# Kernel tuning notes

Measured on AMD Instinct MI355X. Metric: run time of the kernel, lower is better.

## Reference

```python
import jax, jax.numpy as jnp
import numpy as np

FACTOR = 0.2          # rotation/zoom/shift factor (init kwarg)
SCALE = 1.0 / 255.0   # rescale (init kwarg)
TWO_PI = 6.283185307179586
B, H, W, C = 64, 224, 224, 3


def _reflect(i, n):
    # TF fill_mode='reflect' index mapping (symmetric with edge repeat)
    m = jnp.mod(i, 2 * n)
    return jnp.where(m >= n, 2 * n - 1 - m, m)


def _bilinear(img, xs, ys):
    # img [H,W,C]; xs, ys [H,W] = input-space sample coords for each output pixel
    h, w, _ = img.shape
    x0f = jnp.floor(xs)
    y0f = jnp.floor(ys)
    fx = (xs - x0f)[..., None]
    fy = (ys - y0f)[..., None]
    x0 = x0f.astype(jnp.int32)
    y0 = y0f.astype(jnp.int32)
    x0r = _reflect(x0, w); x1r = _reflect(x0 + 1, w)
    y0r = _reflect(y0, h); y1r = _reflect(y0 + 1, h)
    Ia = img[y0r, x0r]; Ib = img[y0r, x1r]
    Ic = img[y1r, x0r]; Id = img[y1r, x1r]
    top = Ia * (1.0 - fx) + Ib * fx
    bot = Ic * (1.0 - fx) + Id * fx
    return top * (1.0 - fy) + bot * fy


_warp = jax.vmap(_bilinear)  # over batch: images [B,H,W,C], coords [B,H,W]


def setup_inputs() -> dict:
    key = jax.random.key(0)
    k = jax.random.split(key, 5)
    return {
        "image": jax.random.uniform(k[0], (B, H, W, C), jnp.float32) * 255.0,
        "angle_u": jax.random.uniform(k[1], (B,), jnp.float32),
        "zoom_u": jax.random.uniform(k[2], (B, 2), jnp.float32),
        "shift_u": jax.random.uniform(k[3], (B, 2), jnp.float32),
        "flip_u": jax.random.uniform(k[4], (B,), jnp.float32),
    }


def reference(image, angle_u, zoom_u, shift_u, flip_u):
    b, h, w, _ = image.shape
    dt = image.dtype
    yy, xx = jnp.meshgrid(jnp.arange(h, dtype=dt), jnp.arange(w, dtype=dt), indexing='ij')
    cx = (w - 1) / 2.0
    cy = (h - 1) / 2.0

    # 1) rescale
    x = image * SCALE

    # 2) random rotation: angle uniform in [-factor*2pi, +factor*2pi]
    theta = (2.0 * angle_u - 1.0) * FACTOR * TWO_PI            # [B]
    c = jnp.cos(theta)[:, None, None]
    s = jnp.sin(theta)[:, None, None]
    xr = c * (xx - cx) - s * (yy - cy) + cx                    # [B,H,W]
    yr = s * (xx - cx) + c * (yy - cy) + cy
    x = _warp(x, xr, yr)

    # 3) random zoom: zoom factor uniform in [1-factor, 1+factor] per axis
    z = 1.0 + (2.0 * zoom_u - 1.0) * FACTOR                    # [B,2] (h, w)
    zh = z[:, 0][:, None, None]
    zw = z[:, 1][:, None, None]
    xz = zw * (xx - cx) + cx
    yz = zh * (yy - cy) + cy
    x = _warp(x, xz, yz)

    # 4) random translation: shift fraction uniform in [-factor, factor]
    sh = (2.0 * shift_u - 1.0) * FACTOR                        # [B,2] (h, w)
    dy = (sh[:, 0] * h)[:, None, None]
    dx = (sh[:, 1] * w)[:, None, None]
    xt = xx - dx
    yt = yy - dy
    x = _warp(x, xt, yt)

    # 5) random horizontal flip (p = 0.5)
    flip = flip_u > 0.5
    x = jnp.where(flip[:, None, None, None], x[:, :, ::-1, :], x)
    return x
```

## Files before the change

kernel.cpp:

```cpp
#include <hip/hip_runtime.h>
#include <hip/hip_fp16.h>
#include <math.h>

#define BB 64
#define HH 224
#define WW 224
#define CC 3

constexpr float FACTOR  = 0.2f;
constexpr float SCALE_K = 1.0f / 255.0f;
constexpr float TWO_PI_F = 6.283185307179586f;
constexpr float CX = (WW - 1) * 0.5f;
constexpr float CY = (HH - 1) * 0.5f;
constexpr int PIX = HH * WW;
constexpr int IMG_ELEMS = PIX * CC;

constexpr int TILES_X = WW / 16;
constexpr int TILES_Y = HH / 16;
constexpr int TILES_PER_IMG = TILES_X * TILES_Y;
constexpr int NXCD = 8;
constexpr int NBLOCKS = BB * TILES_PER_IMG;

__device__ __forceinline__ int reflect1(int i, int n) {
    i = (i < 0) ? (-1 - i) : i;
    return (i >= n) ? (2 * n - 1 - i) : i;
}

__device__ __forceinline__ void decode_tile(int bid, int& b, int& tx, int& ty) {
    int xcd  = bid & (NXCD - 1);
    int slot = bid >> 3;
    int bi   = slot / TILES_PER_IMG;
    int t    = slot - bi * TILES_PER_IMG;
    b = xcd + bi * NXCD;
    ty = t / TILES_X;
    tx = t - ty * TILES_X;
}

__device__ __forceinline__ void unpack_px(uint2 v, float* o) {
    o[0] = __half2float(__ushort_as_half((unsigned short)(v.x & 0xffffu)));
    o[1] = __half2float(__ushort_as_half((unsigned short)(v.x >> 16)));
    o[2] = __half2float(__ushort_as_half((unsigned short)(v.y & 0xffffu)));
}

__global__ __launch_bounds__(256)
void rotate_kernel(const float* __restrict__ image, uint2* __restrict__ tmp,
                   const float* __restrict__ angle_u) {
    int b, tx, ty;
    decode_tile(blockIdx.x, b, tx, ty);
    const int x = tx * 16 + (threadIdx.x & 15);
    const int y = ty * 16 + (threadIdx.x >> 4);

    float theta = (2.0f * angle_u[b] - 1.0f) * FACTOR * TWO_PI_F;
    float c = cosf(theta), s = sinf(theta);

    float rx = (float)x - CX;
    float ry = (float)y - CY;
    float xs = c * rx - s * ry + CX;
    float ys = s * rx + c * ry + CY;

    float x0f = floorf(xs), y0f = floorf(ys);
    float fx = xs - x0f, fy = ys - y0f;
    int x0 = (int)x0f, y0 = (int)y0f;
    int x0r = reflect1(x0,     WW);
    int x1r = reflect1(x0 + 1, WW);
    int y0r = reflect1(y0,     HH);
    int y1r = reflect1(y0 + 1, HH);

    const float* img = image + (size_t)b * IMG_ELEMS;
    const float* Ia = img + (y0r * WW + x0r) * CC;
    const float* Ib = img + (y0r * WW + x1r) * CC;
    const float* Ic = img + (y1r * WW + x0r) * CC;
    const float* Id = img + (y1r * WW + x1r) * CC;

    const float omfx = 1.0f - fx;
    const float omfy = 1.0f - fy;

    float o[3];
#pragma unroll
    for (int ch = 0; ch < CC; ++ch) {
        float top = Ia[ch] * omfx + Ib[ch] * fx;
        float bot = Ic[ch] * omfx + Id[ch] * fx;
        o[ch] = (top * omfy + bot * fy) * SCALE_K;
    }

    unsigned u0 = __half_as_ushort(__float2half_rn(o[0]));
    unsigned u1 = __half_as_ushort(__float2half_rn(o[1]));
    unsigned u2 = __half_as_ushort(__float2half_rn(o[2]));
    uint2 v;
    v.x = u0 | (u1 << 16);
    v.y = u2;
    tmp[(size_t)b * PIX + y * WW + x] = v;
}

__global__ __launch_bounds__(256)
void zoomshift_kernel(const uint2* __restrict__ tmp, float* __restrict__ out,
                      const float* __restrict__ zoom_u,
                      const float* __restrict__ shift_u,
                      const float* __restrict__ flip_u) {
    int b, tx, ty;
    decode_tile(blockIdx.x, b, tx, ty);

    const float zh = 1.0f + (2.0f * zoom_u[2 * b + 0] - 1.0f) * FACTOR;
    const float zw = 1.0f + (2.0f * zoom_u[2 * b + 1] - 1.0f) * FACTOR;
    const float dy = ((2.0f * shift_u[2 * b + 0] - 1.0f) * FACTOR) * (float)HH;
    const float dx = ((2.0f * shift_u[2 * b + 1] - 1.0f) * FACTOR) * (float)WW;
    const bool flip = flip_u[b] > 0.5f;

    const float ndxf = floorf(-dx), ndyf = floorf(-dy);
    const int Kx = (int)ndxf, Ky = (int)ndyf;
    const float fx3 = -dx - ndxf;
    const float fy3 = -dy - ndyf;

    const int Xmin = (flip ? (WW - 16 - tx * 16) : tx * 16) + Kx;
    const int Ymin = ty * 16 + Ky;

    __shared__ float Z[17 * 17 * 3];

    const uint2* img = tmp + (size_t)b * PIX;

    for (int e = threadIdx.x; e < 17 * 17; e += 256) {
        int ey = e / 17;
        int ex = e - ey * 17;
        int Yr = reflect1(Ymin + ey, HH);
        int Xr = reflect1(Xmin + ex, WW);

        float ys2 = zh * ((float)Yr - CY) + CY;
        float xs2 = zw * ((float)Xr - CX) + CX;
        float yf = floorf(ys2), xf = floorf(xs2);
        float fy2 = ys2 - yf, fx2 = xs2 - xf;
        int y20 = (int)yf, x20 = (int)xf;
        int r0 = reflect1(y20,     HH);
        int r1 = reflect1(y20 + 1, HH);
        int c0 = reflect1(x20,     WW);
        int c1 = reflect1(x20 + 1, WW);

        uint2 va = img[r0 * WW + c0];
        uint2 vb = img[r0 * WW + c1];
        uint2 vc = img[r1 * WW + c0];
        uint2 vd = img[r1 * WW + c1];
        float A[3], Bv[3], Cv[3], Dv[3];
        unpack_px(va, A); unpack_px(vb, Bv); unpack_px(vc, Cv); unpack_px(vd, Dv);

        const float omfx = 1.0f - fx2, omfy = 1.0f - fy2;
        float* zp = &Z[e * 3];
#pragma unroll
        for (int ch = 0; ch < CC; ++ch) {
            float top = A[ch]  * omfx + Bv[ch] * fx2;
            float bot = Cv[ch] * omfx + Dv[ch] * fx2;
            zp[ch] = top * omfy + bot * fy2;
        }
    }
    __syncthreads();

    const int lx = threadIdx.x & 15, ly = threadIdx.x >> 4;
    const int x = tx * 16 + lx, y = ty * 16 + ly;
    const int ix = flip ? (15 - lx) : lx;
    const int iy = ly;

    const float* z00 = &Z[(iy * 17 + ix) * 3];
    const float* z01 = &Z[(iy * 17 + ix + 1) * 3];
    const float* z10 = &Z[((iy + 1) * 17 + ix) * 3];
    const float* z11 = &Z[((iy + 1) * 17 + ix + 1) * 3];

    float* o = out + ((size_t)b * PIX + (size_t)y * WW + x) * CC;
    const float omfx3 = 1.0f - fx3, omfy3 = 1.0f - fy3;
#pragma unroll
    for (int ch = 0; ch < CC; ++ch) {
        float top = z00[ch] * omfx3 + z01[ch] * fx3;
        float bot = z10[ch] * omfx3 + z11[ch] * fx3;
        o[ch] = top * omfy3 + bot * fy3;
    }
}

extern "C" void kernel_launch(void* const* d_in, const int* in_sizes, int n_in,
                              void* d_out, int out_size, void* d_ws, size_t ws_size,
                              hipStream_t stream) {
    const float* image   = (const float*)d_in[0];
    const float* angle_u = (const float*)d_in[1];
    const float* zoom_u  = (const float*)d_in[2];
    const float* shift_u = (const float*)d_in[3];
    const float* flip_u  = (const float*)d_in[4];
    float* out = (float*)d_out;

    uint2* tmp = (uint2*)d_ws;

    rotate_kernel<<<NBLOCKS, 256, 0, stream>>>(image, tmp, angle_u);
    zoomshift_kernel<<<NBLOCKS, 256, 0, stream>>>(tmp, out, zoom_u, shift_u, flip_u);
}
```

Baseline: 38.44 us.

## Stage source footprints in shared memory for rotate and zoom gathers

Both kernels now compute the reflected bounding box of the source region each 16x16 output tile needs. They load that box cooperatively with vector loads into LDS and then do the bilinear gathers from LDS instead of scattered global loads. The rotate kernel loads a 24x32 float4 window and switches to fast __sinf/__cosf. The zoom kernel loads a 32x32 fp16 window and keeps its intermediate in LDS as packed fp16. Indices are clamped to the window size, so a tile whose footprint exceeds the window (for example under zoom-out or near reflection edges) would silently give wrong samples, and the extra fp16 rounding adds precision risk.

```diff
diff --git a/kernel.cpp b/kernel.cpp
--- a/kernel.cpp
+++ b/kernel.cpp
@@ -16,14 +16,23 @@
 constexpr int IMG_ELEMS = PIX * CC;
 
 constexpr int TILES_X = WW / 16;
-constexpr int TILES_Y = HH / 16;
-constexpr int TILES_PER_IMG = TILES_X * TILES_Y;
+constexpr int TILES_PER_IMG = TILES_X * TILES_X;
 constexpr int NXCD = 8;
 constexpr int NBLOCKS = BB * TILES_PER_IMG;
+
+typedef float f32x4 __attribute__((ext_vector_type(4), aligned(4)));
+typedef unsigned int u32x4 __attribute__((ext_vector_type(4), aligned(8)));
 
 __device__ __forceinline__ int reflect1(int i, int n) {
     i = (i < 0) ? (-1 - i) : i;
     return (i >= n) ? (2 * n - 1 - i) : i;
+}
+
+__device__ __forceinline__ void rhull(int a, int b, int n, int& lo, int& hi) {
+    int ra = reflect1(a, n), rb = reflect1(b, n);
+    lo = min(ra, rb); hi = max(ra, rb);
+    if (a <= 0 && b >= -1) lo = 0;
+    if (b >= n - 1 && a <= n) hi = n - 1;
 }
 
 __device__ __forceinline__ void decode_tile(int bid, int& b, int& tx, int& ty) {
@@ -36,60 +45,81 @@
     tx = t - ty * TILES_X;
 }
 
-__device__ __forceinline__ void unpack_px(uint2 v, float* o) {
+__device__ __forceinline__ void up3(uint2 v, float* o) {
     o[0] = __half2float(__ushort_as_half((unsigned short)(v.x & 0xffffu)));
     o[1] = __half2float(__ushort_as_half((unsigned short)(v.x >> 16)));
     o[2] = __half2float(__ushort_as_half((unsigned short)(v.y & 0xffffu)));
 }
 
+__device__ __forceinline__ uint2 pack3(float a, float b, float c) {
+    uint2 v;
+    v.x = (unsigned)__half_as_ushort(__float2half_rn(a)) |
+          ((unsigned)__half_as_ushort(__float2half_rn(b)) << 16);
+    v.y = (unsigned)__half_as_ushort(__float2half_rn(c));
+    return v;
+}
+
 __global__ __launch_bounds__(256)
 void rotate_kernel(const float* __restrict__ image, uint2* __restrict__ tmp,
                    const float* __restrict__ angle_u) {
+    __shared__ float4 S[24][33];
     int b, tx, ty;
     decode_tile(blockIdx.x, b, tx, ty);
-    const int x = tx * 16 + (threadIdx.x & 15);
-    const int y = ty * 16 + (threadIdx.x >> 4);
-
-    float theta = (2.0f * angle_u[b] - 1.0f) * FACTOR * TWO_PI_F;
-    float c = cosf(theta), s = sinf(theta);
-
-    float rx = (float)x - CX;
-    float ry = (float)y - CY;
-    float xs = c * rx - s * ry + CX;
-    float ys = s * rx + c * ry + CY;
-
-    float x0f = floorf(xs), y0f = floorf(ys);
-    float fx = xs - x0f, fy = ys - y0f;
-    int x0 = (int)x0f, y0 = (int)y0f;
-    int x0r = reflect1(x0,     WW);
-    int x1r = reflect1(x0 + 1, WW);
-    int y0r = reflect1(y0,     HH);
-    int y1r = reflect1(y0 + 1, HH);
+    const int ox = tx * 16, oy = ty * 16;
+
+    const float theta = (2.0f * angle_u[b] - 1.0f) * FACTOR * TWO_PI_F;
+    const float c = __cosf(theta), s = __sinf(theta);
+
+    const float rx0 = (float)ox - CX, rx1 = (float)(ox + 15) - CX;
+    const float ry0 = (float)oy - CY, ry1 = (float)(oy + 15) - CY;
+    const int Xlo = (int)floorf(fminf(c * rx0, c * rx1) + fminf(-s * ry0, -s * ry1) + CX);
+    const int Xhi = (int)floorf(fmaxf(c * rx0, c * rx1) + fmaxf(-s * ry0, -s * ry1) + CX) + 1;
+    const int Ylo = (int)floorf(fminf(s * rx0, s * rx1) + fminf(c * ry0, c * ry1) + CY);
+    const int Yhi = (int)floorf(fmaxf(s * rx0, s * rx1) + fmaxf(c * ry0, c * ry1) + CY) + 1;
+    int Cx0, Cx1, Cy0, Cy1;
+    rhull(Xlo, Xhi, WW, Cx0, Cx1);
+    rhull(Ylo, Yhi, HH, Cy0, Cy1);
 
     const float* img = image + (size_t)b * IMG_ELEMS;
-    const float* Ia = img + (y0r * WW + x0r) * CC;
-    const float* Ib = img + (y0r * WW + x1r) * CC;
-    const float* Ic = img + (y1r * WW + x0r) * CC;
-    const float* Id = img + (y1r * WW + x1r) * CC;
-
-    const float omfx = 1.0f - fx;
-    const float omfy = 1.0f - fy;
-
-    float o[3];
+    {
+        const int lc  = threadIdx.x & 31;
+        const int col = min(Cx0 + lc, WW - 1);
 #pragma unroll
-    for (int ch = 0; ch < CC; ++ch) {
-        float top = Ia[ch] * omfx + Ib[ch] * fx;
-        float bot = Ic[ch] * omfx + Id[ch] * fx;
-        o[ch] = (top * omfy + bot * fy) * SCALE_K;
+        for (int it = 0; it < 3; ++it) {
+            const int r   = it * 8 + (threadIdx.x >> 5);
+            const int row = min(Cy0 + r, HH - 1);
+            int pe = (row * WW + col) * CC;
+            const bool last = pe > IMG_ELEMS - 4;
+            pe = min(pe, IMG_ELEMS - 4);
+            f32x4 v = *(const f32x4*)(img + pe);
+            S[r][lc] = last ? make_float4(v.y, v.z, v.w, 0.0f)
+                            : make_float4(v.x, v.y, v.z, v.w);
+        }
     }
-
-    unsigned u0 = __half_as_ushort(__float2half_rn(o[0]));
-    unsigned u1 = __half_as_ushort(__float2half_rn(o[1]));
-    unsigned u2 = __half_as_ushort(__float2half_rn(o[2]));
-    uint2 v;
-    v.x = u0 | (u1 << 16);
-    v.y = u2;
-    tmp[(size_t)b * PIX + y * WW + x] = v;
+    __syncthreads();
+
+    const int x = ox + (threadIdx.x & 15), y = oy + (threadIdx.x >> 4);
+    const float xs = c * ((float)x - CX) - s * ((float)y - CY) + CX;
+    const float ys = s * ((float)x - CX) + c * ((float)y - CY) + CY;
+    const float xf = floorf(xs), yf = floorf(ys);
+    const float fx = xs - xf, fy = ys - yf;
+    const int x0 = (int)xf, y0 = (int)yf;
+    const int c0 = min(max(reflect1(x0,     WW) - Cx0, 0), 31);
+    const int c1 = min(max(reflect1(x0 + 1, WW) - Cx0, 0), 31);
+    const int r0 = min(max(reflect1(y0,     HH) - Cy0, 0), 23);
+    const int r1 = min(max(reflect1(y0 + 1, HH) - Cy0, 0), 23);
+
+    const float4 A  = S[r0][c0];
+    const float4 Bv = S[r0][c1];
+    const float4 Cv = S[r1][c0];
+    const float4 Dv = S[r1][c1];
+
+    const float ofx = 1.0f - fx, ofy = 1.0f - fy;
+    const float o0 = ((A.x * ofx + Bv.x * fx) * ofy + (Cv.x * ofx + Dv.x * fx) * fy) * SCALE_K;
+    const float o1 = ((A.y * ofx + Bv.y * fx) * ofy + (Cv.y * ofx + Dv.y * fx) * fy) * SCALE_K;
+    const float o2 = ((A.z * ofx + Bv.z * fx) * ofy + (Cv.z * ofx + Dv.z * fx) * fy) * SCALE_K;
+
+    tmp[(size_t)b * PIX + y * WW + x] = pack3(o0, o1, o2);
 }
 
 __global__ __launch_bounds__(256)
@@ -97,8 +127,11 @@
                       const float* __restrict__ zoom_u,
                       const float* __restrict__ shift_u,
                       const float* __restrict__ flip_u) {
+    __shared__ uint2 Sz[32][34];
+    __shared__ uint2 Zl[17][18];
     int b, tx, ty;
     decode_tile(blockIdx.x, b, tx, ty);
+    const int ox = tx * 16, oy = ty * 16;
 
     const float zh = 1.0f + (2.0f * zoom_u[2 * b + 0] - 1.0f) * FACTOR;
     const float zw = 1.0f + (2.0f * zoom_u[2 * b + 1] - 1.0f) * FACTOR;
@@ -108,68 +141,75 @@
 
     const float ndxf = floorf(-dx), ndyf = floorf(-dy);
     const int Kx = (int)ndxf, Ky = (int)ndyf;
-    const float fx3 = -dx - ndxf;
-    const float fy3 = -dy - ndyf;
-
-    const int Xmin = (flip ? (WW - 16 - tx * 16) : tx * 16) + Kx;
-    const int Ymin = ty * 16 + Ky;
-
-    __shared__ float Z[17 * 17 * 3];
-
-    const uint2* img = tmp + (size_t)b * PIX;
-
-    for (int e = threadIdx.x; e < 17 * 17; e += 256) {
-        int ey = e / 17;
-        int ex = e - ey * 17;
-        int Yr = reflect1(Ymin + ey, HH);
-        int Xr = reflect1(Xmin + ex, WW);
-
-        float ys2 = zh * ((float)Yr - CY) + CY;
-        float xs2 = zw * ((float)Xr - CX) + CX;
-        float yf = floorf(ys2), xf = floorf(xs2);
-        float fy2 = ys2 - yf, fx2 = xs2 - xf;
-        int y20 = (int)yf, x20 = (int)xf;
-        int r0 = reflect1(y20,     HH);
-        int r1 = reflect1(y20 + 1, HH);
-        int c0 = reflect1(x20,     WW);
-        int c1 = reflect1(x20 + 1, WW);
-
-        uint2 va = img[r0 * WW + c0];
-        uint2 vb = img[r0 * WW + c1];
-        uint2 vc = img[r1 * WW + c0];
-        uint2 vd = img[r1 * WW + c1];
-        float A[3], Bv[3], Cv[3], Dv[3];
-        unpack_px(va, A); unpack_px(vb, Bv); unpack_px(vc, Cv); unpack_px(vd, Dv);
-
-        const float omfx = 1.0f - fx2, omfy = 1.0f - fy2;
-        float* zp = &Z[e * 3];
+    const float fx3 = -dx - ndxf, fy3 = -dy - ndyf;
+
+    const int Xmin = (flip ? WW - 16 - ox : ox) + Kx;
+    const int Ymin = oy + Ky;
+
+    int XrLo, XrHi, YrLo, YrHi;
+    rhull(Xmin, Xmin + 16, WW, XrLo, XrHi);
+    rhull(Ymin, Ymin + 16, HH, YrLo, YrHi);
+
+    const int Gx0 = (int)floorf(zw * ((float)XrLo - CX) + CX);
+    const int Gx1 = (int)floorf(zw * ((float)XrHi - CX) + CX) + 1;
+    const int Gy0 = (int)floorf(zh * ((float)YrLo - CY) + CY);
+    const int Gy1 = (int)floorf(zh * ((float)YrHi - CY) + CY) + 1;
+    int Cx0, Cx1, Cy0, Cy1;
+    rhull(Gx0, Gx1, WW, Cx0, Cx1);
+    rhull(Gy0, Gy1, HH, Cy0, Cy1);
+    const int CxA = Cx0 & ~1;
+
+    const uint2* timg = tmp + (size_t)b * PIX;
+    {
+        const int cp  = (threadIdx.x & 15) * 2;
+        const int col = min(CxA + cp, WW - 2);
 #pragma unroll
-        for (int ch = 0; ch < CC; ++ch) {
-            float top = A[ch]  * omfx + Bv[ch] * fx2;
-            float bot = Cv[ch] * omfx + Dv[ch] * fx2;
-            zp[ch] = top * omfy + bot * fy2;
+        for (int it = 0; it < 2; ++it) {
+            const int r   = it * 16 + (threadIdx.x >> 4);
+            const int row = min(Cy0 + r, HH - 1);
+            u32x4 v = *(const u32x4*)(timg + row * WW + col);
+            *(u32x4*)(&Sz[r][cp]) = v;
         }
     }
     __syncthreads();
 
+    for (int e = threadIdx.x; e < 17 * 17; e += 256) {
+        const int ey = e / 17, ex = e - ey * 17;
+        const int Xr = reflect1(Xmin + ex, WW);
+        const int Yr = reflect1(Ymin + ey, HH);
+        const float xs2 = zw * ((float)Xr - CX) + CX;
+        const float ys2 = zh * ((float)Yr - CY) + CY;
+        const float xf = floorf(xs2), yf = floorf(ys2);
+        const float fx2 = xs2 - xf, fy2 = ys2 - yf;
+        const int x20 = (int)xf, y20 = (int)yf;
+        const int cA = min(max(reflect1(x20,     WW) - CxA, 0), 31);
+        const int cB = min(max(reflect1(x20 + 1, WW) - CxA, 0), 31);
+        const int rA = min(max(reflect1(y20,     HH) - Cy0, 0), 31);
+        const int rB = min(max(reflect1(y20 + 1, HH) - Cy0, 0), 31);
+
+        float A[3], Bv[3], Cv[3], Dv[3];
+        up3(Sz[rA][cA], A);  up3(Sz[rA][cB], Bv);
+        up3(Sz[rB][cA], Cv); up3(Sz[rB][cB], Dv);
+
+        const float ofx = 1.0f - fx2, ofy = 1.0f - fy2;
+        const float z0 = (A[0] * ofx + Bv[0] * fx2) * ofy + (Cv[0] * ofx + Dv[0] * fx2) * fy2;
+        const float z1 = (A[1] * ofx + Bv[1] * fx2) * ofy + (Cv[1] * ofx + Dv[1] * fx2) * fy2;
+        const float z2 = (A[2] * ofx + Bv[2] * fx2) * ofy + (Cv[2] * ofx + Dv[2] * fx2) * fy2;
+        Zl[ey][ex] = pack3(z0, z1, z2);
+    }
+    __syncthreads();
+
     const int lx = threadIdx.x & 15, ly = threadIdx.x >> 4;
-    const int x = tx * 16 + lx, y = ty * 16 + ly;
     const int ix = flip ? (15 - lx) : lx;
-    const int iy = ly;
-
-    const float* z00 = &Z[(iy * 17 + ix) * 3];
-    const float* z01 = &Z[(iy * 17 + ix + 1) * 3];
-    const float* z10 = &Z[((iy + 1) * 17 + ix) * 3];
-    const float* z11 = &Z[((iy + 1) * 17 + ix + 1) * 3];
-
-    float* o = out + ((size_t)b * PIX + (size_t)y * WW + x) * CC;
-    const float omfx3 = 1.0f - fx3, omfy3 = 1.0f - fy3;
-#pragma unroll
-    for (int ch = 0; ch < CC; ++ch) {
-        float top = z00[ch] * omfx3 + z01[ch] * fx3;
-        float bot = z10[ch] * omfx3 + z11[ch] * fx3;
-        o[ch] = top * omfy3 + bot * fy3;
-    }
+    float A[3], Bv[3], Cv[3], Dv[3];
+    up3(Zl[ly][ix],     A);  up3(Zl[ly][ix + 1],     Bv);
+    up3(Zl[ly + 1][ix], Cv); up3(Zl[ly + 1][ix + 1], Dv);
+
+    float* o = out + ((size_t)b * PIX + (size_t)(oy + ly) * WW + (ox + lx)) * CC;
+    const float ofx = 1.0f - fx3, ofy = 1.0f - fy3;
+    o[0] = (A[0] * ofx + Bv[0] * fx3) * ofy + (Cv[0] * ofx + Dv[0] * fx3) * fy3;
+    o[1] = (A[1] * ofx + Bv[1] * fx3) * ofy + (Cv[1] * ofx + Dv[1] * fx3) * fy3;
+    o[2] = (A[2] * ofx + Bv[2] * fx3) * ofy + (Cv[2] * ofx + Dv[2] * fx3) * fy3;
 }
 
 extern "C" void kernel_launch(void* const* d_in, const int* in_sizes, int n_in,
```

Measured after the change: 42.03 us. 1.09x slower.
